# Optimization experiments

Hardware: AMD Instinct MI355X
Metric: run time of the kernel (lower is better)

## Reference

```python
import jax, jax.numpy as jnp
import numpy as np

N = 50000
E = 800000
NODE_SIZE = 64
NUM_RADIAL = 20
CUTOFF = 5.0


def setup_inputs() -> dict:
    key = jax.random.key(0)
    ks = jax.random.split(key, 12)
    node_scalar = jax.random.normal(ks[0], (N, NODE_SIZE), dtype=jnp.float32)
    node_vector = jax.random.normal(ks[1], (N, 3, NODE_SIZE), dtype=jnp.float32)
    edge = jax.random.randint(ks[2], (E, 2), 0, N, dtype=jnp.int64)
    edge_diff = jax.random.normal(ks[3], (E, 3), dtype=jnp.float32)
    # positive distances in (0, cutoff]; most edges inside cutoff
    edge_dist = jax.random.uniform(ks[4], (E, 1), dtype=jnp.float32) * CUTOFF + 1e-2
    s = 1.0 / np.sqrt(NODE_SIZE)
    r = 1.0 / np.sqrt(NUM_RADIAL)
    W1 = jax.random.normal(ks[5], (NODE_SIZE, NODE_SIZE), dtype=jnp.float32) * s
    b1 = jnp.zeros((NODE_SIZE,), dtype=jnp.float32)
    W2 = jax.random.normal(ks[6], (NODE_SIZE, 3 * NODE_SIZE), dtype=jnp.float32) * s
    b2 = jnp.zeros((3 * NODE_SIZE,), dtype=jnp.float32)
    Wf = jax.random.normal(ks[7], (NUM_RADIAL, 3 * NODE_SIZE), dtype=jnp.float32) * r
    bf = jnp.zeros((3 * NODE_SIZE,), dtype=jnp.float32)
    return {"node_scalar": node_scalar, "node_vector": node_vector, "edge": edge,
            "edge_diff": edge_diff, "edge_dist": edge_dist,
            "W1": W1, "b1": b1, "W2": W2, "b2": b2, "Wf": Wf, "bf": bf}


def reference(node_scalar, node_vector, edge, edge_diff, edge_dist, W1, b1, W2, b2, Wf, bf):
    S = NODE_SIZE
    n_nodes = node_scalar.shape[0]
    # sinc radial basis: sin(n*pi*d/cutoff)/d, n=1..num_radial -> [E, R]
    n = jnp.arange(1, NUM_RADIAL + 1, dtype=edge_dist.dtype)
    rbf = jnp.sin(edge_dist * n * jnp.pi / CUTOFF) / edge_dist
    filter_weight = rbf @ Wf + bf                       # [E, 3S]
    # cosine cutoff, broadcast [E,1] over [E,3S]
    cut = jnp.where(edge_dist < CUTOFF,
                    0.5 * (jnp.cos(jnp.pi * edge_dist / CUTOFF) + 1.0),
                    jnp.zeros((), edge_dist.dtype))
    filter_weight = filter_weight * cut
    # scalar message MLP on nodes: Linear -> SiLU -> Linear
    scalar_out = jax.nn.silu(node_scalar @ W1 + b1) @ W2 + b2   # [N, 3S]
    src = edge[:, 1]
    dst = edge[:, 0]
    filter_out = filter_weight * scalar_out[src]        # [E, 3S]
    gate_state_vector = filter_out[:, :S]
    gate_edge_vector = filter_out[:, S:2 * S]
    message_scalar = filter_out[:, 2 * S:]
    unit = (edge_diff / edge_dist)[:, :, None]          # [E, 3, 1]
    message_vector = node_vector[src] * gate_state_vector[:, None, :] + gate_edge_vector[:, None, :] * unit  # [E,3,S]
    residual_scalar = jax.ops.segment_sum(message_scalar, dst, num_segments=n_nodes)
    residual_vector = jax.ops.segment_sum(message_vector, dst, num_segments=n_nodes)
    return node_scalar + residual_scalar, node_vector + residual_vector
```

## Files before the change

### kernel.cpp

```cpp
#include <hip/hip_runtime.h>
#include <hip/hip_bf16.h>
#include <math.h>

#define N_NODES 50000
#define N_EDGES 800000
#define NRAD 20
#define NBLK 196
#define CAP 48

typedef short bf16x8 __attribute__((ext_vector_type(8)));
typedef float f32x4 __attribute__((ext_vector_type(4)));
typedef _Float16 half2v __attribute__((ext_vector_type(2)));
typedef int i32x16 __attribute__((ext_vector_type(16)));

__device__ __forceinline__ unsigned short f2b(float f) {
    union { __hip_bfloat16 h; unsigned short u; } cv;
    cv.h = __float2bfloat16(f);
    return cv.u;
}
__device__ __forceinline__ unsigned int packh2(float a, float b) {
    union { _Float16 h; unsigned short u; } A, B;
    A.h = (_Float16)a; B.h = (_Float16)b;
    return (unsigned int)A.u | ((unsigned int)B.u << 16);
}
__device__ __forceinline__ half2v ash2u(unsigned int x) {
    union { unsigned int u; half2v h; } u; u.u = x; return u.h;
}
__device__ __forceinline__ f32x4 mfma16(bf16x8 a, bf16x8 b, f32x4 c) {
    return __builtin_amdgcn_mfma_f32_16x16x32_bf16(a, b, c, 0, 0, 0);
}

__global__ __launch_bounds__(256) void prep0_kernel(
    int* __restrict__ counts,
    const float* __restrict__ W1, const float* __restrict__ W2, const float* __restrict__ Wf,
    unsigned short* __restrict__ W1t, unsigned short* __restrict__ W2t,
    unsigned int* __restrict__ Wfp) {
    int i = blockIdx.x * 256 + threadIdx.x;
    if (i < N_NODES) counts[i] = 0;
    if (i < 192 * 64) {
        int n = i >> 6, k = i & 63;
        W2t[i] = f2b(W2[k * 192 + n]);
        if (i < 64 * 64) W1t[i] = f2b(W1[k * 64 + n]);
        if (i < 1920) {
            int ch = i / 640, rem = i % 640, j = rem >> 6, l = rem & 63;
            Wfp[i] = packh2(Wf[(2 * j) * 192 + ch * 64 + l],
                            Wf[(2 * j + 1) * 192 + ch * 64 + l]);
        }
    }
}

__global__ void hist_kernel(const int2* __restrict__ edge2, int* __restrict__ counts) {
    int e = blockIdx.x * blockDim.x + threadIdx.x;
    if (e < N_EDGES) atomicAdd(&counts[edge2[e].x], 1);
}

__global__ __launch_bounds__(256) void scanall_kernel(const int* __restrict__ counts,
                                                      int* __restrict__ offs,
                                                      int* __restrict__ cursors) {
    __shared__ int ss[256];
    int t = threadIdx.x, b = blockIdx.x;
    int lim = b * 256;
    int s = 0;
    for (int i = t; i < lim; i += 256) s += counts[i];
    ss[t] = s;
    __syncthreads();
    for (int k = 128; k > 0; k >>= 1) {
        if (t < k) ss[t] += ss[t + k];
        __syncthreads();
    }
    int base0 = ss[0];
    __syncthreads();
    int i = lim + t;
    int v = (i < N_NODES) ? counts[i] : 0;
    ss[t] = v;
    __syncthreads();
    for (int off = 1; off < 256; off <<= 1) {
        int u = (t >= off) ? ss[t - off] : 0;
        __syncthreads();
        ss[t] += u;
        __syncthreads();
    }
    int excl = base0 + ss[t] - v;
    if (i < N_NODES) {
        offs[i] = excl;
        cursors[i] = excl;
    }
    if (i == N_NODES - 1) offs[N_NODES] = excl + v;
}

template <int C>
__global__ __launch_bounds__(256) void bucket_kernel(
    const int2* __restrict__ edge2, const float* __restrict__ ediff,
    const float* __restrict__ edist, int* __restrict__ cursors,
    float4* __restrict__ pack) {
    int e = blockIdx.x * blockDim.x + threadIdx.x;
    if (e >= N_EDGES) return;
    int2 ed = edge2[e];
    int slot = atomicAdd(&cursors[ed.x], 1);
    size_t pos;
    if (C > 0) {
        if (slot >= C) return;
        pos = (size_t)ed.x * C + slot;
    } else {
        pos = (size_t)slot;
    }
    int src = ed.y;

    float dist = edist[e];
    float d0 = ediff[3 * e], d1 = ediff[3 * e + 1], d2 = ediff[3 * e + 2];
    float inv = __builtin_amdgcn_rcpf(dist);
    float x = dist * (3.14159265358979323846f / 5.0f);
    float s1 = __sinf(x);
    float c1 = __cosf(x);
    float cut = (dist < 5.0f) ? 0.5f * (c1 + 1.0f) : 0.0f;
    float ic = inv * cut;
    float t2 = 2.0f * c1;
    float r[NRAD];
    float sn = s1, sp = 0.0f;
#pragma unroll
    for (int k = 0; k < NRAD; k++) {
        r[k] = sn * ic;
        float nx = t2 * sn - sp;
        sp = sn;
        sn = nx;
    }
    unsigned int rp[10];
#pragma unroll
    for (int j = 0; j < 10; j++) rp[j] = packh2(r[2 * j], r[2 * j + 1]);

    float4* P = pack + pos * 4;
    P[0] = make_float4(__int_as_float(src), cut, d0 * inv, d1 * inv);
    P[1] = make_float4(d2 * inv, __uint_as_float(rp[0]), __uint_as_float(rp[1]),
                       __uint_as_float(rp[2]));
    P[2] = make_float4(__uint_as_float(rp[3]), __uint_as_float(rp[4]),
                       __uint_as_float(rp[5]), __uint_as_float(rp[6]));
    P[3] = make_float4(__uint_as_float(rp[7]), __uint_as_float(rp[8]),
                       __uint_as_float(rp[9]), 0.0f);
}

__global__ __launch_bounds__(256) void node_mlp_kernel(
    const float* __restrict__ ns, const float* __restrict__ nv,
    const unsigned short* __restrict__ W1t, const float* __restrict__ b1,
    const unsigned short* __restrict__ W2t, const float* __restrict__ b2,
    unsigned short* __restrict__ snb) {
    __shared__ unsigned short LB[64 * 200];
    unsigned short* H = LB;
    unsigned short* O = LB;
    int t = threadIdx.x;
    int lane = t & 63;
    int w = t >> 6;
    int c15 = lane & 15;
    int quad = lane >> 4;
    int base = blockIdx.x * 64;

    int node = base + 16 * w + c15;
    if (node >= N_NODES) node = N_NODES - 1;

    bf16x8 a0, a1;
    {
        const float* xr = ns + (size_t)node * 64 + quad * 8;
        float4 p0 = *(const float4*)xr;
        float4 p1 = *(const float4*)(xr + 4);
        float4 p2 = *(const float4*)(xr + 32);
        float4 p3 = *(const float4*)(xr + 36);
        a0[0] = (short)f2b(p0.x); a0[1] = (short)f2b(p0.y);
        a0[2] = (short)f2b(p0.z); a0[3] = (short)f2b(p0.w);
        a0[4] = (short)f2b(p1.x); a0[5] = (short)f2b(p1.y);
        a0[6] = (short)f2b(p1.z); a0[7] = (short)f2b(p1.w);
        a1[0] = (short)f2b(p2.x); a1[1] = (short)f2b(p2.y);
        a1[2] = (short)f2b(p2.z); a1[3] = (short)f2b(p2.w);
        a1[4] = (short)f2b(p3.x); a1[5] = (short)f2b(p3.y);
        a1[6] = (short)f2b(p3.z); a1[7] = (short)f2b(p3.w);
    }

#pragma unroll
    for (int nt = 0; nt < 4; nt++) {
        float bc = b1[nt * 16 + c15];
        f32x4 acc = {bc, bc, bc, bc};
        bf16x8 w0 = *(const bf16x8*)(W1t + (nt * 16 + c15) * 64 + quad * 8);
        bf16x8 w1 = *(const bf16x8*)(W1t + (nt * 16 + c15) * 64 + 32 + quad * 8);
        acc = mfma16(a0, w0, acc);
        acc = mfma16(a1, w1, acc);
#pragma unroll
        for (int r = 0; r < 4; r++) {
            float v = acc[r];
            v = v / (1.0f + __expf(-v));
            H[(16 * w + quad * 4 + r) * 72 + nt * 16 + c15] = f2b(v);
        }
    }

    bf16x8 h0 = *(const bf16x8*)(H + (16 * w + c15) * 72 + quad * 8);
    bf16x8 h1 = *(const bf16x8*)(H + (16 * w + c15) * 72 + 32 + quad * 8);
    __syncthreads();

#pragma unroll
    for (int nt = 0; nt < 12; nt++) {
        float bc = b2[nt * 16 + c15];
        f32x4 acc = {bc, bc, bc, bc};
        bf16x8 w0 = *(const bf16x8*)(W2t + (nt * 16 + c15) * 64 + quad * 8);
        bf16x8 w1 = *(const bf16x8*)(W2t + (nt * 16 + c15) * 64 + 32 + quad * 8);
        acc = mfma16(h0, w0, acc);
        acc = mfma16(h1, w1, acc);
#pragma unroll
        for (int r = 0; r < 4; r++)
            O[(16 * w + quad * 4 + r) * 200 + nt * 16 + c15] = f2b(acc[r]);
    }
    __syncthreads();

    int nb = min(64, N_NODES - base);
    for (int idx = t; idx < nb * 64; idx += 256) {
        int row = idx >> 6, ll = idx & 63;
        unsigned short o0 = O[row * 200 + ll];
        unsigned short o1 = O[row * 200 + 64 + ll];
        unsigned short o2 = O[row * 200 + 128 + ll];
        int nd = base + row;
        float v0 = nv[(size_t)nd * 192 + ll];
        float v1 = nv[(size_t)nd * 192 + 64 + ll];
        float v2 = nv[(size_t)nd * 192 + 128 + ll];
        uint3 pkv;
        pkv.x = (unsigned int)o0 | ((unsigned int)o1 << 16);
        pkv.y = (unsigned int)o2 | ((unsigned int)f2b(v0) << 16);
        pkv.z = (unsigned int)f2b(v1) | ((unsigned int)f2b(v2) << 16);
        *(uint3*)((char*)snb + (size_t)nd * 768 + ll * 12) = pkv;
    }
}

template <int C>
__global__ __launch_bounds__(256) void gather_kernel(
    const float* __restrict__ ns, const float* __restrict__ nv,
    const unsigned int* __restrict__ Wfp, const float* __restrict__ bfv,
    const unsigned short* __restrict__ snb, const int* __restrict__ offs,
    const float4* __restrict__ pack, float* __restrict__ out0, float* __restrict__ out1) {
    int t = threadIdx.x;
    int l = t & 63;
    int wid = __builtin_amdgcn_readfirstlane((int)(blockIdx.x * 4 + (t >> 6)));
    int W = gridDim.x * 4;

    half2v wf0[10], wf1[10], wf2[10];
#pragma unroll
    for (int j = 0; j < 10; j++) {
        wf0[j] = ash2u(Wfp[j * 64 + l]);
        wf1[j] = ash2u(Wfp[640 + j * 64 + l]);
        wf2[j] = ash2u(Wfp[1280 + j * 64 + l]);
    }
    float bf0 = bfv[l], bf1 = bfv[64 + l], bf2 = bfv[128 + l];

    const char* packb = (const char*)pack;
    const char* snbb = (const char*)snb;

    for (int n = wid; n < N_NODES; n += W) {
        int start, end;
        if (C > 0) {
            start = n * C;
            int c = __builtin_amdgcn_readfirstlane(offs[n]);
            if (c > C) c = C;
            end = start + c;
        } else {
            start = __builtin_amdgcn_readfirstlane(offs[n]);
            end = __builtin_amdgcn_readfirstlane(offs[n + 1]);
        }
        float acc_s = 0.0f, a0 = 0.0f, a1 = 0.0f, a2 = 0.0f;

        if (start < end) {
            i32x16 A;
            unsigned long long pa =
                (unsigned long long)packb + (unsigned long long)(unsigned)start * 64ull;
            asm volatile("s_load_dwordx16 %0, %1, 0x0" : "=s"(A) : "s"(pa));
            asm volatile("s_waitcnt lgkmcnt(0)" : "+s"(A));
            i32x16 B = A;
            uint3 gA = *(const uint3*)(snbb + (size_t)(unsigned)A[0] * 768 + l * 12);
            if (start + 1 < end)
                asm volatile("s_load_dwordx16 %0, %1, 0x0" : "=s"(B) : "s"(pa + 64ull));

            for (int i = start; i < end; i++) {
                float cut = __int_as_float(A[1]);
                float u0 = __int_as_float(A[2]);
                float u1 = __int_as_float(A[3]);
                float u2 = __int_as_float(A[4]);
                float f0 = bf0 * cut, f1 = bf1 * cut, f2 = bf2 * cut;
#pragma unroll
                for (int j = 0; j < 10; j++) {
                    half2v rp = ash2u((unsigned)A[5 + j]);
                    f0 = __builtin_amdgcn_fdot2(rp, wf0[j], f0, false);
                    f1 = __builtin_amdgcn_fdot2(rp, wf1[j], f1, false);
                    f2 = __builtin_amdgcn_fdot2(rp, wf2[j], f2, false);
                }
                uint3 gN = gA;
                if (i + 1 < end) {
                    asm volatile("s_waitcnt lgkmcnt(0)" : "+s"(B));
                    gN = *(const uint3*)(snbb + (size_t)(unsigned)B[0] * 768 + l * 12);
                }
                float s0 = __uint_as_float(gA.x << 16);
                float s1 = __uint_as_float(gA.x & 0xffff0000u);
                float s2 = __uint_as_float(gA.y << 16);
                float v0 = __uint_as_float(gA.y & 0xffff0000u);
                float v1 = __uint_as_float(gA.z << 16);
                float v2 = __uint_as_float(gA.z & 0xffff0000u);
                float gg0 = f0 * s0, gg1 = f1 * s1;
                acc_s += f2 * s2;
                a0 += fmaf(v0, gg0, gg1 * u0);
                a1 += fmaf(v1, gg0, gg1 * u1);
                a2 += fmaf(v2, gg0, gg1 * u2);
                A = B;
                gA = gN;
                if (i + 2 < end) {
                    unsigned long long pn =
                        (unsigned long long)packb + (unsigned long long)(unsigned)(i + 2) * 64ull;
                    asm volatile("s_load_dwordx16 %0, %1, 0x0" : "=s"(B) : "s"(pn));
                }
            }
        }

        size_t b64 = (size_t)n * 64 + l, b192 = (size_t)n * 192 + l;
        out0[b64] = ns[b64] + acc_s;
        out1[b192] = nv[b192] + a0;
        out1[b192 + 64] = nv[b192 + 64] + a1;
        out1[b192 + 128] = nv[b192 + 128] + a2;
    }
}

extern "C" void kernel_launch(void* const* d_in, const int* in_sizes, int n_in,
                              void* d_out, int out_size, void* d_ws, size_t ws_size,
                              hipStream_t stream) {
    const float* ns    = (const float*)d_in[0];
    const float* nv    = (const float*)d_in[1];
    const int2*  edge2 = (const int2*)d_in[2];
    const float* ediff = (const float*)d_in[3];
    const float* edist = (const float*)d_in[4];
    const float* W1    = (const float*)d_in[5];
    const float* b1    = (const float*)d_in[6];
    const float* W2    = (const float*)d_in[7];
    const float* b2    = (const float*)d_in[8];
    const float* Wf    = (const float*)d_in[9];
    const float* bfv   = (const float*)d_in[10];

    float* out0 = (float*)d_out;
    float* out1 = out0 + (size_t)N_NODES * 64;

    const size_t cap_pack = (size_t)N_NODES * CAP * 64;
    const size_t need_cap = cap_pack + (size_t)N_NODES * 768 + 8192 + 24576 + 7680 +
                            (size_t)N_NODES * 4 + 4096;
    bool capmode = ws_size >= need_cap;

    char* wsp = (char*)d_ws;
    float4* pack = (float4*)wsp;
    wsp += capmode ? cap_pack : (size_t)N_EDGES * 64;
    unsigned short* snb = (unsigned short*)wsp;     wsp += (size_t)N_NODES * 768;
    unsigned short* W1t = (unsigned short*)wsp;     wsp += 64 * 64 * 2;
    unsigned short* W2t = (unsigned short*)wsp;     wsp += 192 * 64 * 2;
    unsigned int* Wfp = (unsigned int*)wsp;         wsp += 1920 * 4;
    int* counts  = (int*)wsp;
    int* offs    = counts + N_NODES;
    int* cursors = offs + (N_NODES + 1);

    if (capmode) {
        prep0_kernel<<<NBLK, 256, 0, stream>>>(counts, W1, W2, Wf, W1t, W2t, Wfp);
        bucket_kernel<CAP><<<(N_EDGES + 255) / 256, 256, 0, stream>>>(edge2, ediff, edist,
                                                                      counts, pack);
        node_mlp_kernel<<<(N_NODES + 63) / 64, 256, 0, stream>>>(ns, nv, W1t, b1, W2t, b2,
                                                                 snb);
        gather_kernel<CAP><<<2048, 256, 0, stream>>>(ns, nv, Wfp, bfv, snb, counts, pack,
                                                     out0, out1);
    } else {
        prep0_kernel<<<NBLK, 256, 0, stream>>>(counts, W1, W2, Wf, W1t, W2t, Wfp);
        hist_kernel<<<(N_EDGES + 255) / 256, 256, 0, stream>>>(edge2, counts);
        scanall_kernel<<<NBLK, 256, 0, stream>>>(counts, offs, cursors);
        bucket_kernel<0><<<(N_EDGES + 255) / 256, 256, 0, stream>>>(edge2, ediff, edist,
                                                                    cursors, pack);
        node_mlp_kernel<<<(N_NODES + 63) / 64, 256, 0, stream>>>(ns, nv, W1t, b1, W2t, b2,
                                                                 snb);
        gather_kernel<0><<<2048, 256, 0, stream>>>(ns, nv, Wfp, bfv, snb, offs, pack,
                                                   out0, out1);
    }
}
```

Measured before the change: 319.5 us.

## Deepen gather prefetch, add atomic work queue, use nontemporal memory ops

The gather loop now keeps a three-deep prefetch of edge records and source-node rows, where it previously kept two, to hide more gather latency. Nodes are handed to waves through a global atomic counter instead of a fixed stride, which balances uneven per-node edge counts. Loads and stores in the bucket and output phases use nontemporal hints to avoid polluting cache. In exchange it costs one extra atomic per node, holds more scalar registers, and waits with a full lgkmcnt(0) each iteration, which can stall on the loads still in flight.

```diff
diff --git a/kernel.cpp b/kernel.cpp
--- a/kernel.cpp
+++ b/kernel.cpp
@@ -12,6 +12,7 @@
 typedef float f32x4 __attribute__((ext_vector_type(4)));
 typedef _Float16 half2v __attribute__((ext_vector_type(2)));
 typedef int i32x16 __attribute__((ext_vector_type(16)));
+typedef int i32x2 __attribute__((ext_vector_type(2)));
 
 __device__ __forceinline__ unsigned short f2b(float f) {
     union { __hip_bfloat16 h; unsigned short u; } cv;
@@ -29,14 +30,18 @@
 __device__ __forceinline__ f32x4 mfma16(bf16x8 a, bf16x8 b, f32x4 c) {
     return __builtin_amdgcn_mfma_f32_16x16x32_bf16(a, b, c, 0, 0, 0);
 }
+__device__ __forceinline__ f32x4 mkv4(float x, float y, float z, float w) {
+    f32x4 v; v[0] = x; v[1] = y; v[2] = z; v[3] = w; return v;
+}
 
 __global__ __launch_bounds__(256) void prep0_kernel(
-    int* __restrict__ counts,
+    int* __restrict__ counts, int* __restrict__ qctr,
     const float* __restrict__ W1, const float* __restrict__ W2, const float* __restrict__ Wf,
     unsigned short* __restrict__ W1t, unsigned short* __restrict__ W2t,
     unsigned int* __restrict__ Wfp) {
     int i = blockIdx.x * 256 + threadIdx.x;
     if (i < N_NODES) counts[i] = 0;
+    if (i == 0) qctr[0] = 0;
     if (i < 192 * 64) {
         int n = i >> 6, k = i & 63;
         W2t[i] = f2b(W2[k * 192 + n]);
@@ -95,19 +100,22 @@
     float4* __restrict__ pack) {
     int e = blockIdx.x * blockDim.x + threadIdx.x;
     if (e >= N_EDGES) return;
-    int2 ed = edge2[e];
-    int slot = atomicAdd(&cursors[ed.x], 1);
+    i32x2 edv = __builtin_nontemporal_load((const i32x2*)&edge2[e]);
+    int dst = edv[0];
+    int src = edv[1];
+    int slot = atomicAdd(&cursors[dst], 1);
     size_t pos;
     if (C > 0) {
         if (slot >= C) return;
-        pos = (size_t)ed.x * C + slot;
+        pos = (size_t)dst * C + slot;
     } else {
         pos = (size_t)slot;
     }
-    int src = ed.y;
-
-    float dist = edist[e];
-    float d0 = ediff[3 * e], d1 = ediff[3 * e + 1], d2 = ediff[3 * e + 2];
+
+    float dist = __builtin_nontemporal_load(&edist[e]);
+    float d0 = __builtin_nontemporal_load(&ediff[3 * e]);
+    float d1 = __builtin_nontemporal_load(&ediff[3 * e + 1]);
+    float d2 = __builtin_nontemporal_load(&ediff[3 * e + 2]);
     float inv = __builtin_amdgcn_rcpf(dist);
     float x = dist * (3.14159265358979323846f / 5.0f);
     float s1 = __sinf(x);
@@ -128,14 +136,18 @@
 #pragma unroll
     for (int j = 0; j < 10; j++) rp[j] = packh2(r[2 * j], r[2 * j + 1]);
 
-    float4* P = pack + pos * 4;
-    P[0] = make_float4(__int_as_float(src), cut, d0 * inv, d1 * inv);
-    P[1] = make_float4(d2 * inv, __uint_as_float(rp[0]), __uint_as_float(rp[1]),
-                       __uint_as_float(rp[2]));
-    P[2] = make_float4(__uint_as_float(rp[3]), __uint_as_float(rp[4]),
-                       __uint_as_float(rp[5]), __uint_as_float(rp[6]));
-    P[3] = make_float4(__uint_as_float(rp[7]), __uint_as_float(rp[8]),
-                       __uint_as_float(rp[9]), 0.0f);
+    f32x4* P = (f32x4*)(pack + pos * 4);
+    __builtin_nontemporal_store(
+        mkv4(__int_as_float(src), cut, d0 * inv, d1 * inv), P + 0);
+    __builtin_nontemporal_store(
+        mkv4(d2 * inv, __uint_as_float(rp[0]), __uint_as_float(rp[1]),
+             __uint_as_float(rp[2])), P + 1);
+    __builtin_nontemporal_store(
+        mkv4(__uint_as_float(rp[3]), __uint_as_float(rp[4]),
+             __uint_as_float(rp[5]), __uint_as_float(rp[6])), P + 2);
+    __builtin_nontemporal_store(
+        mkv4(__uint_as_float(rp[7]), __uint_as_float(rp[8]),
+             __uint_as_float(rp[9]), 0.0f), P + 3);
 }
 
 __global__ __launch_bounds__(256) void node_mlp_kernel(
@@ -230,11 +242,10 @@
     const float* __restrict__ ns, const float* __restrict__ nv,
     const unsigned int* __restrict__ Wfp, const float* __restrict__ bfv,
     const unsigned short* __restrict__ snb, const int* __restrict__ offs,
-    const float4* __restrict__ pack, float* __restrict__ out0, float* __restrict__ out1) {
+    const float4* __restrict__ pack, float* __restrict__ out0, float* __restrict__ out1,
+    int* __restrict__ qctr) {
     int t = threadIdx.x;
     int l = t & 63;
-    int wid = __builtin_amdgcn_readfirstlane((int)(blockIdx.x * 4 + (t >> 6)));
-    int W = gridDim.x * 4;
 
     half2v wf0[10], wf1[10], wf2[10];
 #pragma unroll
@@ -248,7 +259,13 @@
     const char* packb = (const char*)pack;
     const char* snbb = (const char*)snb;
 
-    for (int n = wid; n < N_NODES; n += W) {
+    int tk = 0;
+    if (l == 0) tk = atomicAdd(qctr, 1);
+    int n = __builtin_amdgcn_readfirstlane(tk);
+
+    while (n < N_NODES) {
+        if (l == 0) tk = atomicAdd(qctr, 1);
+
         int start, end;
         if (C > 0) {
             start = n * C;
@@ -262,60 +279,72 @@
         float acc_s = 0.0f, a0 = 0.0f, a1 = 0.0f, a2 = 0.0f;
 
         if (start < end) {
-            i32x16 A;
+            i32x16 P0, P1, P2;
             unsigned long long pa =
                 (unsigned long long)packb + (unsigned long long)(unsigned)start * 64ull;
-            asm volatile("s_load_dwordx16 %0, %1, 0x0" : "=s"(A) : "s"(pa));
-            asm volatile("s_waitcnt lgkmcnt(0)" : "+s"(A));
-            i32x16 B = A;
-            uint3 gA = *(const uint3*)(snbb + (size_t)(unsigned)A[0] * 768 + l * 12);
-            if (start + 1 < end)
-                asm volatile("s_load_dwordx16 %0, %1, 0x0" : "=s"(B) : "s"(pa + 64ull));
-
+            asm volatile("s_load_dwordx16 %0, %1, 0x0" : "=s"(P0) : "s"(pa));
+            asm volatile("s_waitcnt lgkmcnt(0)" : "+s"(P0));
+            uint3 g0 = *(const uint3*)(snbb + (size_t)(unsigned)P0[0] * 768 + l * 12);
+            P1 = P0; P2 = P0;
+            uint3 g1 = g0;
+            if (start + 1 < end) {
+                asm volatile("s_load_dwordx16 %0, %1, 0x0" : "=s"(P1) : "s"(pa + 64ull));
+                asm volatile("s_waitcnt lgkmcnt(0)" : "+s"(P1));
+                g1 = *(const uint3*)(snbb + (size_t)(unsigned)P1[0] * 768 + l * 12);
+                if (start + 2 < end)
+                    asm volatile("s_load_dwordx16 %0, %1, 0x0" : "=s"(P2) : "s"(pa + 128ull));
+            }
+            uint3 gn = g0;
             for (int i = start; i < end; i++) {
-                float cut = __int_as_float(A[1]);
-                float u0 = __int_as_float(A[2]);
-                float u1 = __int_as_float(A[3]);
-                float u2 = __int_as_float(A[4]);
+                if (i + 2 < end) {
+                    asm volatile("s_waitcnt lgkmcnt(0)" : "+s"(P2));
+                    gn = *(const uint3*)(snbb + (size_t)(unsigned)P2[0] * 768 + l * 12);
+                }
+                float cut = __int_as_float(P0[1]);
+                float u0 = __int_as_float(P0[2]);
+                float u1 = __int_as_float(P0[3]);
+                float u2 = __int_as_float(P0[4]);
                 float f0 = bf0 * cut, f1 = bf1 * cut, f2 = bf2 * cut;
 #pragma unroll
                 for (int j = 0; j < 10; j++) {
-                    half2v rp = ash2u((unsigned)A[5 + j]);
+                    half2v rp = ash2u((unsigned)P0[5 + j]);
                     f0 = __builtin_amdgcn_fdot2(rp, wf0[j], f0, false);
                     f1 = __builtin_amdgcn_fdot2(rp, wf1[j], f1, false);
                     f2 = __builtin_amdgcn_fdot2(rp, wf2[j], f2, false);
                 }
-                uint3 gN = gA;
-                if (i + 1 < end) {
-                    asm volatile("s_waitcnt lgkmcnt(0)" : "+s"(B));
-                    gN = *(const uint3*)(snbb + (size_t)(unsigned)B[0] * 768 + l * 12);
-                }
-                float s0 = __uint_as_float(gA.x << 16);
-                float s1 = __uint_as_float(gA.x & 0xffff0000u);
-                float s2 = __uint_as_float(gA.y << 16);
-                float v0 = __uint_as_float(gA.y & 0xffff0000u);
-                float v1 = __uint_as_float(gA.z << 16);
-                float v2 = __uint_as_float(gA.z & 0xffff0000u);
+                float s0 = __uint_as_float(g0.x << 16);
+                float s1 = __uint_as_float(g0.x & 0xffff0000u);
+                float s2 = __uint_as_float(g0.y << 16);
+                float v0 = __uint_as_float(g0.y & 0xffff0000u);
+                float v1 = __uint_as_float(g0.z << 16);
+                float v2 = __uint_as_float(g0.z & 0xffff0000u);
                 float gg0 = f0 * s0, gg1 = f1 * s1;
                 acc_s += f2 * s2;
                 a0 += fmaf(v0, gg0, gg1 * u0);
                 a1 += fmaf(v1, gg0, gg1 * u1);
                 a2 += fmaf(v2, gg0, gg1 * u2);
-                A = B;
-                gA = gN;
-                if (i + 2 < end) {
+                P0 = P1; P1 = P2;
+                g0 = g1; g1 = gn;
+                if (i + 3 < end) {
                     unsigned long long pn =
-                        (unsigned long long)packb + (unsigned long long)(unsigned)(i + 2) * 64ull;
-                    asm volatile("s_load_dwordx16 %0, %1, 0x0" : "=s"(B) : "s"(pn));
+                        (unsigned long long)packb +
+                        (unsigned long long)(unsigned)(i + 3) * 64ull;
+                    asm volatile("s_load_dwordx16 %0, %1, 0x0" : "=s"(P2) : "s"(pn));
                 }
             }
         }
 
         size_t b64 = (size_t)n * 64 + l, b192 = (size_t)n * 192 + l;
-        out0[b64] = ns[b64] + acc_s;
-        out1[b192] = nv[b192] + a0;
-        out1[b192 + 64] = nv[b192 + 64] + a1;
-        out1[b192 + 128] = nv[b192 + 128] + a2;
+        __builtin_nontemporal_store(
+            __builtin_nontemporal_load(ns + b64) + acc_s, out0 + b64);
+        __builtin_nontemporal_store(
+            __builtin_nontemporal_load(nv + b192) + a0, out1 + b192);
+        __builtin_nontemporal_store(
+            __builtin_nontemporal_load(nv + b192 + 64) + a1, out1 + b192 + 64);
+        __builtin_nontemporal_store(
+            __builtin_nontemporal_load(nv + b192 + 128) + a2, out1 + b192 + 128);
+
+        n = __builtin_amdgcn_readfirstlane(tk);
     }
 }
 
@@ -352,17 +381,18 @@
     int* counts  = (int*)wsp;
     int* offs    = counts + N_NODES;
     int* cursors = offs + (N_NODES + 1);
+    int* qctr = capmode ? (counts + N_NODES) : (cursors + N_NODES);
 
     if (capmode) {
-        prep0_kernel<<<NBLK, 256, 0, stream>>>(counts, W1, W2, Wf, W1t, W2t, Wfp);
+        prep0_kernel<<<NBLK, 256, 0, stream>>>(counts, qctr, W1, W2, Wf, W1t, W2t, Wfp);
         bucket_kernel<CAP><<<(N_EDGES + 255) / 256, 256, 0, stream>>>(edge2, ediff, edist,
                                                                       counts, pack);
         node_mlp_kernel<<<(N_NODES + 63) / 64, 256, 0, stream>>>(ns, nv, W1t, b1, W2t, b2,
                                                                  snb);
         gather_kernel<CAP><<<2048, 256, 0, stream>>>(ns, nv, Wfp, bfv, snb, counts, pack,
-                                                     out0, out1);
+                                                     out0, out1, qctr);
     } else {
-        prep0_kernel<<<NBLK, 256, 0, stream>>>(counts, W1, W2, Wf, W1t, W2t, Wfp);
+        prep0_kernel<<<NBLK, 256, 0, stream>>>(counts, qctr, W1, W2, Wf, W1t, W2t, Wfp);
         hist_kernel<<<(N_EDGES + 255) / 256, 256, 0, stream>>>(edge2, counts);
         scanall_kernel<<<NBLK, 256, 0, stream>>>(counts, offs, cursors);
         bucket_kernel<0><<<(N_EDGES + 255) / 256, 256, 0, stream>>>(edge2, ediff, edist,
@@ -370,6 +400,6 @@
         node_mlp_kernel<<<(N_NODES + 63) / 64, 256, 0, stream>>>(ns, nv, W1t, b1, W2t, b2,
                                                                  snb);
         gather_kernel<0><<<2048, 256, 0, stream>>>(ns, nv, Wfp, bfv, snb, offs, pack,
-                                                   out0, out1);
-    }
-}
+                                                   out0, out1, qctr);
+    }
+}
```

Measured after the change: 940.5 us. +194.4%, slower.
